# Kernel optimization log

Hardware: AMD Instinct MI355X
Metric: run time of the kernel (lower is better)

Reference implementation:

```python
import jax, jax.numpy as jnp
import numpy as np

N = 200000
E = 1000000
IN_DIM = 16
HID = 64
OUT = 1
EPS = 1e-5


def setup_inputs() -> dict:
    key = jax.random.key(0)
    ks = jax.random.split(key, 24)
    x = jax.random.normal(ks[0], (N, IN_DIM), dtype=jnp.float32)
    edge_index = jax.random.randint(ks[1], (2, E), 0, N, dtype=jnp.int64)

    def lin(k, fan_in, fan_out):
        s = 1.0 / np.sqrt(fan_in)
        return jax.random.uniform(k, (fan_in, fan_out), jnp.float32, -s, s)

    inp = {
        'x': x, 'edge_index': edge_index,
        'W1': lin(ks[2], IN_DIM, HID), 'b1': jnp.zeros((HID,), jnp.float32),
        'W2': lin(ks[3], HID, HID), 'b2': jnp.zeros((HID,), jnp.float32),
        'W3': lin(ks[4], HID, HID), 'b3': jnp.zeros((HID,), jnp.float32),
        'fc_w': lin(ks[5], HID, OUT),
        'fc_b': jnp.zeros((OUT,), jnp.float32),
    }
    # BatchNorm params / running stats (eval mode) — randomized for nontrivial math
    for i, kk in zip((1, 2, 3), range(6, 24, 4)):
        inp[f'g{i}'] = 1.0 + 0.1 * jax.random.normal(ks[kk], (HID,), jnp.float32)
        inp[f'be{i}'] = 0.1 * jax.random.normal(ks[kk + 1], (HID,), jnp.float32)
        inp[f'm{i}'] = 0.1 * jax.random.normal(ks[kk + 2], (HID,), jnp.float32)
        inp[f'v{i}'] = 0.5 + jax.random.uniform(ks[kk + 3], (HID,), jnp.float32)
    return inp


def gcn_conv(x, src, dst, W, b):
    # PyG GCNConv: add self-loops, symmetric normalization, aggregate at dst, bias after aggregation
    h = x @ W                                   # [N, F]
    deg = 1.0 + jax.ops.segment_sum(jnp.ones((E,), x.dtype), dst, num_segments=N)
    dinv = jax.lax.rsqrt(deg)                   # deg >= 1 (self loop)
    norm = dinv[src] * dinv[dst]                # [E]
    msg = h[src] * norm[:, None]                # [E, F] gather + scale
    agg = jax.ops.segment_sum(msg, dst, num_segments=N)
    agg = agg + h * (dinv * dinv)[:, None]      # self-loop contribution
    return agg + b


def bn(x, g, be, m, v):
    return g * (x - m) * jax.lax.rsqrt(v + EPS) + be


def reference(x, edge_index, W1, b1, W2, b2, W3, b3, fc_w, fc_b,
              g1, be1, m1, v1, g2, be2, m2, v2, g3, be3, m3, v3):
    src, dst = edge_index[0], edge_index[1]
    h = jax.nn.relu(bn(gcn_conv(x, src, dst, W1, b1), g1, be1, m1, v1))
    residual = h  # dropout is identity in eval mode
    h = jax.nn.relu(bn(gcn_conv(h, src, dst, W2, b2), g2, be2, m2, v2))
    h = jax.nn.relu(bn(gcn_conv(h, src, dst, W3, b3), g3, be3, m3, v3))
    h = h + residual
    out = h @ fc_w + fc_b
    return jax.nn.sigmoid(out) * 10.0
```

## Files before the change

kernel.cpp:

```cpp
#include <hip/hip_runtime.h>
#include <hip/hip_bf16.h>
#include <math.h>

constexpr int HIDF = 64;

typedef __attribute__((ext_vector_type(8))) short short8;
typedef __attribute__((ext_vector_type(4))) float f32x4;

static inline size_t align_up(size_t x, size_t a) { return (x + a - 1) & ~(a - 1); }

__device__ inline ushort f2bf(float x) {
    __hip_bfloat16 h = __float2bfloat16(x);
    return __builtin_bit_cast(ushort, h);
}
__device__ inline float bflo(unsigned int u) {
    return __builtin_bit_cast(float, u << 16);
}
__device__ inline float bfhi(unsigned int u) {
    return __builtin_bit_cast(float, u & 0xffff0000u);
}
__device__ inline unsigned int pack2(float lo, float hi) {
    return (unsigned int)f2bf(lo) | ((unsigned int)f2bf(hi) << 16);
}


__global__ __launch_bounds__(256) void k_hist(const int* __restrict__ dst,
                                              int* __restrict__ bukcnt,
                                              int ne, int nbuk) {
    __shared__ int lh[512];
    int tid = threadIdx.x;
    lh[tid] = 0; lh[tid + 256] = 0;
    __syncthreads();
#pragma unroll
    for (int k = 0; k < 8; ++k) {
        int idx = blockIdx.x * 2048 + k * 256 + tid;
        if (idx < ne) atomicAdd(&lh[dst[idx] >> 9], 1);
    }
    __syncthreads();
    for (int b = tid; b < nbuk; b += 256) {
        int c = lh[b];
        if (c) atomicAdd(&bukcnt[b], c);
    }
}

__global__ __launch_bounds__(512) void k_bukscan(const int* __restrict__ bukcnt,
                                                 int* __restrict__ bukbase,
                                                 int* __restrict__ gcur,
                                                 int* __restrict__ rowptr,
                                                 int nbuk, int ne, int n) {
    __shared__ int s[512];
    int tid = threadIdx.x;
    int c = (tid < nbuk) ? bukcnt[tid] : 0;
    s[tid] = c;
    __syncthreads();
    for (int off = 1; off < 512; off <<= 1) {
        int t = (tid >= off) ? s[tid - off] : 0;
        __syncthreads();
        s[tid] += t;
        __syncthreads();
    }
    int excl = s[tid] - c;
    if (tid < nbuk) { bukbase[tid] = excl; gcur[tid * 16] = excl; }
    if (tid == 0) { bukbase[nbuk] = ne; rowptr[n] = ne; }
}

__global__ __launch_bounds__(256) void k_scatter_pairs(
    const int* __restrict__ src, const int* __restrict__ dst,
    int* __restrict__ gcur, unsigned* __restrict__ pairs, int ne, int nbuk) {
    __shared__ int lh[512];
    __shared__ int lb[512];
    int tid = threadIdx.x;
    int d[16], sv[16];
#pragma unroll
    for (int k = 0; k < 16; ++k) {
        int idx = blockIdx.x * 4096 + k * 256 + tid;
        bool ok = idx < ne;
        d[k] = ok ? dst[idx] : -1;
        sv[k] = ok ? src[idx] : 0;
    }
    lh[tid] = 0; lh[tid + 256] = 0;
    __syncthreads();
#pragma unroll
    for (int k = 0; k < 16; ++k)
        if (d[k] >= 0) atomicAdd(&lh[d[k] >> 9], 1);
    __syncthreads();
    for (int b = tid; b < nbuk; b += 256) {
        int c = lh[b];
        lb[b] = c ? atomicAdd(&gcur[b * 16], c) : 0;
    }
    __syncthreads();
#pragma unroll
    for (int k = 0; k < 16; ++k)
        if (d[k] >= 0) {
            int pos = atomicAdd(&lb[d[k] >> 9], 1);
            pairs[pos] = (unsigned)sv[k] | ((unsigned)(d[k] & 511) << 18);
        }
}

__global__ __launch_bounds__(512) void k_bucket_sort(
    const unsigned* __restrict__ pairs, const int* __restrict__ bukbase,
    int* __restrict__ rowptr, float* __restrict__ dinv,
    int* __restrict__ esrc, int n) {
    __shared__ int lcnt[512];
    __shared__ int lscan[512];
    __shared__ int lcur[512];
    __shared__ int stage[4096];
    int b = blockIdx.x, tid = threadIdx.x;
    int base = bukbase[b];
    int cnt = bukbase[b + 1] - base;
    lcnt[tid] = 0;
    __syncthreads();
    for (int i = tid; i < cnt; i += 512)
        atomicAdd(&lcnt[pairs[base + i] >> 18], 1);
    __syncthreads();
    int v = lcnt[tid];
    lscan[tid] = v;
    __syncthreads();
    for (int off = 1; off < 512; off <<= 1) {
        int t = (tid >= off) ? lscan[tid - off] : 0;
        __syncthreads();
        lscan[tid] += t;
        __syncthreads();
    }
    int excl = lscan[tid] - v;
    lcur[tid] = excl;
    int node = (b << 9) + tid;
    if (node < n) {
        rowptr[node] = base + excl;
        dinv[node] = rsqrtf(1.f + (float)v);
    }
    __syncthreads();
    for (int i = tid; i < cnt; i += 512) {
        unsigned u = pairs[base + i];
        int p = atomicAdd(&lcur[u >> 18], 1);
        if (p < 4096) stage[p] = (int)(u & 0x3FFFF);
    }
    __syncthreads();
    for (int i = tid; i < cnt && i < 4096; i += 512)
        esrc[base + i] = stage[i];
}

__global__ __launch_bounds__(256) void k_prep(
    const float* __restrict__ W1, const float* __restrict__ W2,
    const float* __restrict__ W3, ushort* __restrict__ wb,
    const float* __restrict__ b1, const float* __restrict__ g1,
    const float* __restrict__ be1, const float* __restrict__ m1, const float* __restrict__ v1,
    const float* __restrict__ b2, const float* __restrict__ g2,
    const float* __restrict__ be2, const float* __restrict__ m2, const float* __restrict__ v2,
    const float* __restrict__ b3, const float* __restrict__ g3,
    const float* __restrict__ be3, const float* __restrict__ m3, const float* __restrict__ v3,
    float* __restrict__ ST) {
    int i = blockIdx.x * 256 + threadIdx.x;
    if (i < 1024) wb[i] = f2bf(W1[i]);
    else if (i < 5120) wb[i] = f2bf(W2[i - 1024]);
    else if (i < 9216) wb[i] = f2bf(W3[i - 5120]);
    int j = i - 9216;
    if (j >= 0 && j < 192) {
        int li = j >> 6, f = j & 63;
        const float* g  = li == 0 ? g1  : li == 1 ? g2  : g3;
        const float* be = li == 0 ? be1 : li == 1 ? be2 : be3;
        const float* m  = li == 0 ? m1  : li == 1 ? m2  : m3;
        const float* v  = li == 0 ? v1  : li == 1 ? v2  : v3;
        const float* bb = li == 0 ? b1  : li == 1 ? b2  : b3;
        float sc = g[f] * rsqrtf(v[f] + 1e-5f);
        ST[li * 128 + f] = sc;
        ST[li * 128 + 64 + f] = sc * (bb[f] - m[f]) + be[f];
    }
}

__global__ __launch_bounds__(256) void k_gemm1(
    const float* __restrict__ X, const ushort* __restrict__ Wb,
    const float* __restrict__ dinv, ushort* __restrict__ hsb, int n) {
    int wid = (blockIdx.x * 256 + threadIdx.x) >> 6;
    int lane = threadIdx.x & 63;
    int lr = lane & 15, lg = lane >> 4;
    int row16 = wid * 16;
    if (row16 >= n) return;

    short8 bf[4];
#pragma unroll
    for (int nt = 0; nt < 4; ++nt) {
        short8 f = {0, 0, 0, 0, 0, 0, 0, 0};
        if (lg < 2)
#pragma unroll
            for (int i = 0; i < 8; ++i)
                f[i] = (short)Wb[(lg * 8 + i) * 64 + nt * 16 + lr];
        bf[nt] = f;
    }

    short8 af = {0, 0, 0, 0, 0, 0, 0, 0};
    if (lg < 2) {
        const float* ar = X + (size_t)(row16 + lr) * 16 + lg * 8;
        float4 u0 = *reinterpret_cast<const float4*>(ar);
        float4 u1 = *reinterpret_cast<const float4*>(ar + 4);
        af[0] = (short)f2bf(u0.x); af[1] = (short)f2bf(u0.y);
        af[2] = (short)f2bf(u0.z); af[3] = (short)f2bf(u0.w);
        af[4] = (short)f2bf(u1.x); af[5] = (short)f2bf(u1.y);
        af[6] = (short)f2bf(u1.z); af[7] = (short)f2bf(u1.w);
    }

    f32x4 acc[4] = {{0, 0, 0, 0}, {0, 0, 0, 0}, {0, 0, 0, 0}, {0, 0, 0, 0}};
#pragma unroll
    for (int nt = 0; nt < 4; ++nt)
        acc[nt] = __builtin_amdgcn_mfma_f32_16x16x32_bf16(af, bf[nt], acc[nt], 0, 0, 0);

#pragma unroll
    for (int j = 0; j < 4; ++j) {
        int row = row16 + lg * 4 + j;
        float di = dinv[row];
#pragma unroll
        for (int nt = 0; nt < 4; ++nt)
            hsb[(size_t)row * 64 + nt * 16 + lr] = f2bf(acc[nt][j] * di);
    }
}

__device__ inline void addrow(float a[8], uint4 u) {
    a[0] += bflo(u.x); a[1] += bfhi(u.x);
    a[2] += bflo(u.y); a[3] += bfhi(u.y);
    a[4] += bflo(u.z); a[5] += bfhi(u.z);
    a[6] += bflo(u.w); a[7] += bfhi(u.w);
}

__device__ inline void agg_core(const uint4* hs4, const int* rowptr,
                                const int* esrc, int node, int q, int lane,
                                float a[8]) {
    addrow(a, hs4[(size_t)node * 8 + q]);
    int start = rowptr[node], deg = rowptr[node + 1] - start;
    int gb = lane & 56;
    int ev = (q < deg) ? esrc[start + q] : 0;
    int it = 0;
    for (; it + 4 <= deg; it += 4) {
        int s0 = (it + 0 < 8) ? __shfl(ev, gb + it + 0, 64) : esrc[start + it + 0];
        int s1 = (it + 1 < 8) ? __shfl(ev, gb + it + 1, 64) : esrc[start + it + 1];
        int s2 = (it + 2 < 8) ? __shfl(ev, gb + it + 2, 64) : esrc[start + it + 2];
        int s3 = (it + 3 < 8) ? __shfl(ev, gb + it + 3, 64) : esrc[start + it + 3];
        uint4 r0 = hs4[(size_t)s0 * 8 + q];
        uint4 r1 = hs4[(size_t)s1 * 8 + q];
        uint4 r2 = hs4[(size_t)s2 * 8 + q];
        uint4 r3 = hs4[(size_t)s3 * 8 + q];
        addrow(a, r0); addrow(a, r1); addrow(a, r2); addrow(a, r3);
    }
    for (; it < deg; ++it) {
        int s = (it < 8) ? __shfl(ev, gb + it, 64) : esrc[start + it];
        addrow(a, hs4[(size_t)s * 8 + q]);
    }
}

template <bool WRITE_H>
__global__ __launch_bounds__(256) void k_agg_gemm(
    const ushort* __restrict__ hsbIn, const int* __restrict__ rowptr,
    const int* __restrict__ esrc, const float* __restrict__ dinv,
    const float* __restrict__ S, const float* __restrict__ T,
    const ushort* __restrict__ Wb, ushort* __restrict__ hb_out,
    ushort* __restrict__ hs_out, int n) {
    __shared__ uint4 hl[8 * 32];
    int tid = threadIdx.x;
    int lane = tid & 63;
    int node0 = blockIdx.x * 32;
    int ln = tid >> 3;
    int node = node0 + ln;
    int q = tid & 7;

    uint4 w = make_uint4(0u, 0u, 0u, 0u);
    if (node < n) {
        float a[8] = {0, 0, 0, 0, 0, 0, 0, 0};
        agg_core(reinterpret_cast<const uint4*>(hsbIn), rowptr, esrc, node, q, lane, a);
        float di = dinv[node];
        const float4* S4 = reinterpret_cast<const float4*>(S);
        const float4* T4 = reinterpret_cast<const float4*>(T);
        float4 sA = S4[q * 2], sB = S4[q * 2 + 1];
        float4 tA = T4[q * 2], tB = T4[q * 2 + 1];
        float o0 = fmaxf(fmaf(sA.x * di, a[0], tA.x), 0.f);
        float o1 = fmaxf(fmaf(sA.y * di, a[1], tA.y), 0.f);
        float o2 = fmaxf(fmaf(sA.z * di, a[2], tA.z), 0.f);
        float o3 = fmaxf(fmaf(sA.w * di, a[3], tA.w), 0.f);
        float o4 = fmaxf(fmaf(sB.x * di, a[4], tB.x), 0.f);
        float o5 = fmaxf(fmaf(sB.y * di, a[5], tB.y), 0.f);
        float o6 = fmaxf(fmaf(sB.z * di, a[6], tB.z), 0.f);
        float o7 = fmaxf(fmaf(sB.w * di, a[7], tB.w), 0.f);
        w.x = pack2(o0, o1); w.y = pack2(o2, o3);
        w.z = pack2(o4, o5); w.w = pack2(o6, o7);
        if (WRITE_H)
            reinterpret_cast<uint4*>(hb_out)[(size_t)node * 8 + q] = w;
    }
    hl[q * 32 + ln] = w;
    __syncthreads();

    int wv = tid >> 6;
    int wr = wv >> 1, wc = wv & 1;
    int lr = lane & 15, lg = lane >> 4;

    short8 af[2];
#pragma unroll
    for (int kt = 0; kt < 2; ++kt)
        af[kt] = __builtin_bit_cast(short8, hl[(kt * 4 + lg) * 32 + wr * 16 + lr]);

    short8 bf[2][2];
#pragma unroll
    for (int nt = 0; nt < 2; ++nt)
#pragma unroll
        for (int kt = 0; kt < 2; ++kt) {
            short8 f;
#pragma unroll
            for (int i = 0; i < 8; ++i)
                f[i] = (short)Wb[(kt * 32 + lg * 8 + i) * 64 + wc * 32 + nt * 16 + lr];
            bf[nt][kt] = f;
        }

    f32x4 acc[2] = {{0, 0, 0, 0}, {0, 0, 0, 0}};
#pragma unroll
    for (int kt = 0; kt < 2; ++kt)
#pragma unroll
        for (int nt = 0; nt < 2; ++nt)
            acc[nt] = __builtin_amdgcn_mfma_f32_16x16x32_bf16(af[kt], bf[nt][kt], acc[nt], 0, 0, 0);

#pragma unroll
    for (int j = 0; j < 4; ++j) {
        int row = node0 + wr * 16 + lg * 4 + j;
        if (row < n) {
            float di = dinv[row];
#pragma unroll
            for (int nt = 0; nt < 2; ++nt)
                hs_out[(size_t)row * 64 + wc * 32 + nt * 16 + lr] = f2bf(acc[nt][j] * di);
        }
    }
}

__global__ __launch_bounds__(256) void k_agg_final(
    const ushort* __restrict__ hsb, const int* __restrict__ rowptr,
    const int* __restrict__ esrc, const float* __restrict__ dinv,
    const float* __restrict__ S, const float* __restrict__ T,
    const ushort* __restrict__ h1, const float* __restrict__ fcw,
    const float* __restrict__ fcb, float* __restrict__ out, int n) {
    int t = blockIdx.x * 256 + threadIdx.x;
    int node = t >> 3;
    if (node >= n) return;
    int q = t & 7, lane = threadIdx.x & 63;
    float a[8] = {0, 0, 0, 0, 0, 0, 0, 0};
    agg_core(reinterpret_cast<const uint4*>(hsb), rowptr, esrc, node, q, lane, a);
    float di = dinv[node];
    const float4* S4 = reinterpret_cast<const float4*>(S);
    const float4* T4 = reinterpret_cast<const float4*>(T);
    float4 sA = S4[q * 2], sB = S4[q * 2 + 1];
    float4 tA = T4[q * 2], tB = T4[q * 2 + 1];
    uint4 r = reinterpret_cast<const uint4*>(h1)[(size_t)node * 8 + q];
    float h0 = fmaxf(fmaf(sA.x * di, a[0], tA.x), 0.f) + bflo(r.x);
    float h1v = fmaxf(fmaf(sA.y * di, a[1], tA.y), 0.f) + bfhi(r.x);
    float h2 = fmaxf(fmaf(sA.z * di, a[2], tA.z), 0.f) + bflo(r.y);
    float h3 = fmaxf(fmaf(sA.w * di, a[3], tA.w), 0.f) + bfhi(r.y);
    float h4 = fmaxf(fmaf(sB.x * di, a[4], tB.x), 0.f) + bflo(r.z);
    float h5 = fmaxf(fmaf(sB.y * di, a[5], tB.y), 0.f) + bfhi(r.z);
    float h6 = fmaxf(fmaf(sB.z * di, a[6], tB.z), 0.f) + bflo(r.w);
    float h7 = fmaxf(fmaf(sB.w * di, a[7], tB.w), 0.f) + bfhi(r.w);
    float4 fA = reinterpret_cast<const float4*>(fcw)[q * 2];
    float4 fB = reinterpret_cast<const float4*>(fcw)[q * 2 + 1];
    float p = h0 * fA.x + h1v * fA.y + h2 * fA.z + h3 * fA.w +
              h4 * fB.x + h5 * fB.y + h6 * fB.z + h7 * fB.w;
    p += __shfl_xor(p, 1, 64);
    p += __shfl_xor(p, 2, 64);
    p += __shfl_xor(p, 4, 64);
    if (q == 0) out[node] = 10.f / (1.f + expf(-(p + fcb[0])));
}

extern "C" void kernel_launch(void* const* d_in, const int* in_sizes, int n_in,
                              void* d_out, int out_size, void* d_ws, size_t ws_size,
                              hipStream_t stream) {
    const float* x   = (const float*)d_in[0];
    const int*   ei  = (const int*)d_in[1];
    const float* W1  = (const float*)d_in[2];
    const float* b1  = (const float*)d_in[3];
    const float* W2  = (const float*)d_in[4];
    const float* b2  = (const float*)d_in[5];
    const float* W3  = (const float*)d_in[6];
    const float* b3  = (const float*)d_in[7];
    const float* fcw = (const float*)d_in[8];
    const float* fcb = (const float*)d_in[9];
    const float* g1 = (const float*)d_in[10], *be1 = (const float*)d_in[11];
    const float* m1 = (const float*)d_in[12], *v1  = (const float*)d_in[13];
    const float* g2 = (const float*)d_in[14], *be2 = (const float*)d_in[15];
    const float* m2 = (const float*)d_in[16], *v2  = (const float*)d_in[17];
    const float* g3 = (const float*)d_in[18], *be3 = (const float*)d_in[19];
    const float* m3 = (const float*)d_in[20], *v3  = (const float*)d_in[21];

    const int N = in_sizes[0] / 16;
    const int E = in_sizes[1] / 2;
    const int* src = ei;
    const int* dst = ei + E;
    float* out = (float*)d_out;

    char* w = (char*)d_ws;
    auto take = [&](size_t bytes) { char* p = w; w += align_up(bytes, 256); return p; };
    float*    dinv    = (float*)take((size_t)N * 4);
    int*      rowptr  = (int*)take((size_t)(N + 1) * 4);
    int*      bukcnt  = (int*)take(512 * 4);
    int*      bukbase = (int*)take(513 * 4);
    int*      gcur    = (int*)take(512 * 16 * 4);
    unsigned* pairs   = (unsigned*)take((size_t)E * 4);
    int*      esrc    = (int*)take((size_t)E * 4);
    ushort*   hsbA    = (ushort*)take((size_t)N * HIDF * 2);
    ushort*   hsbB    = (ushort*)take((size_t)N * HIDF * 2);
    ushort*   h1b     = (ushort*)take((size_t)N * HIDF * 2);
    ushort*   wb      = (ushort*)take((size_t)9216 * 2);
    float*    ST      = (float*)take(3 * 128 * 4);

    const int NBUK  = (N + 511) >> 9;
    const int gHist = (E + 2047) / 2048;
    const int gScat = (E + 4095) / 4096;
    const int gT    = ((N + 15) / 16 * 64 + 255) / 256;
    const int gAG   = (N + 31) / 32;
    const int gAgg  = (N * 8 + 255) / 256;

    hipMemsetAsync(bukcnt, 0, 512 * 4, stream);
    k_hist<<<gHist, 256, 0, stream>>>(dst, bukcnt, E, NBUK);
    k_bukscan<<<1, 512, 0, stream>>>(bukcnt, bukbase, gcur, rowptr, NBUK, E, N);
    k_scatter_pairs<<<gScat, 256, 0, stream>>>(src, dst, gcur, pairs, E, NBUK);
    k_bucket_sort<<<NBUK, 512, 0, stream>>>(pairs, bukbase, rowptr, dinv, esrc, N);

    k_prep<<<37, 256, 0, stream>>>(W1, W2, W3, wb,
                                   b1, g1, be1, m1, v1,
                                   b2, g2, be2, m2, v2,
                                   b3, g3, be3, m3, v3, ST);

    k_gemm1<<<gT, 256, 0, stream>>>(x, wb, dinv, hsbA, N);
    k_agg_gemm<true><<<gAG, 256, 0, stream>>>(hsbA, rowptr, esrc, dinv,
                                              ST, ST + 64, wb + 1024, h1b, hsbB, N);
    k_agg_gemm<false><<<gAG, 256, 0, stream>>>(hsbB, rowptr, esrc, dinv,
                                               ST + 128, ST + 192, wb + 5120, nullptr, hsbA, N);
    k_agg_final<<<gAgg, 256, 0, stream>>>(hsbA, rowptr, esrc, dinv,
                                          ST + 256, ST + 320, h1b, fcw, fcb, out, N);
}
```

Baseline: 255.0 us.

## Fuse weight prep into histogram, vectorize edge loads, add occupancy bounds

```diff
diff --git a/kernel.cpp b/kernel.cpp
--- a/kernel.cpp
+++ b/kernel.cpp
@@ -24,123 +24,8 @@
 }
 
 
-__global__ __launch_bounds__(256) void k_hist(const int* __restrict__ dst,
-                                              int* __restrict__ bukcnt,
-                                              int ne, int nbuk) {
-    __shared__ int lh[512];
-    int tid = threadIdx.x;
-    lh[tid] = 0; lh[tid + 256] = 0;
-    __syncthreads();
-#pragma unroll
-    for (int k = 0; k < 8; ++k) {
-        int idx = blockIdx.x * 2048 + k * 256 + tid;
-        if (idx < ne) atomicAdd(&lh[dst[idx] >> 9], 1);
-    }
-    __syncthreads();
-    for (int b = tid; b < nbuk; b += 256) {
-        int c = lh[b];
-        if (c) atomicAdd(&bukcnt[b], c);
-    }
-}
-
-__global__ __launch_bounds__(512) void k_bukscan(const int* __restrict__ bukcnt,
-                                                 int* __restrict__ bukbase,
-                                                 int* __restrict__ gcur,
-                                                 int* __restrict__ rowptr,
-                                                 int nbuk, int ne, int n) {
-    __shared__ int s[512];
-    int tid = threadIdx.x;
-    int c = (tid < nbuk) ? bukcnt[tid] : 0;
-    s[tid] = c;
-    __syncthreads();
-    for (int off = 1; off < 512; off <<= 1) {
-        int t = (tid >= off) ? s[tid - off] : 0;
-        __syncthreads();
-        s[tid] += t;
-        __syncthreads();
-    }
-    int excl = s[tid] - c;
-    if (tid < nbuk) { bukbase[tid] = excl; gcur[tid * 16] = excl; }
-    if (tid == 0) { bukbase[nbuk] = ne; rowptr[n] = ne; }
-}
-
-__global__ __launch_bounds__(256) void k_scatter_pairs(
-    const int* __restrict__ src, const int* __restrict__ dst,
-    int* __restrict__ gcur, unsigned* __restrict__ pairs, int ne, int nbuk) {
-    __shared__ int lh[512];
-    __shared__ int lb[512];
-    int tid = threadIdx.x;
-    int d[16], sv[16];
-#pragma unroll
-    for (int k = 0; k < 16; ++k) {
-        int idx = blockIdx.x * 4096 + k * 256 + tid;
-        bool ok = idx < ne;
-        d[k] = ok ? dst[idx] : -1;
-        sv[k] = ok ? src[idx] : 0;
-    }
-    lh[tid] = 0; lh[tid + 256] = 0;
-    __syncthreads();
-#pragma unroll
-    for (int k = 0; k < 16; ++k)
-        if (d[k] >= 0) atomicAdd(&lh[d[k] >> 9], 1);
-    __syncthreads();
-    for (int b = tid; b < nbuk; b += 256) {
-        int c = lh[b];
-        lb[b] = c ? atomicAdd(&gcur[b * 16], c) : 0;
-    }
-    __syncthreads();
-#pragma unroll
-    for (int k = 0; k < 16; ++k)
-        if (d[k] >= 0) {
-            int pos = atomicAdd(&lb[d[k] >> 9], 1);
-            pairs[pos] = (unsigned)sv[k] | ((unsigned)(d[k] & 511) << 18);
-        }
-}
-
-__global__ __launch_bounds__(512) void k_bucket_sort(
-    const unsigned* __restrict__ pairs, const int* __restrict__ bukbase,
-    int* __restrict__ rowptr, float* __restrict__ dinv,
-    int* __restrict__ esrc, int n) {
-    __shared__ int lcnt[512];
-    __shared__ int lscan[512];
-    __shared__ int lcur[512];
-    __shared__ int stage[4096];
-    int b = blockIdx.x, tid = threadIdx.x;
-    int base = bukbase[b];
-    int cnt = bukbase[b + 1] - base;
-    lcnt[tid] = 0;
-    __syncthreads();
-    for (int i = tid; i < cnt; i += 512)
-        atomicAdd(&lcnt[pairs[base + i] >> 18], 1);
-    __syncthreads();
-    int v = lcnt[tid];
-    lscan[tid] = v;
-    __syncthreads();
-    for (int off = 1; off < 512; off <<= 1) {
-        int t = (tid >= off) ? lscan[tid - off] : 0;
-        __syncthreads();
-        lscan[tid] += t;
-        __syncthreads();
-    }
-    int excl = lscan[tid] - v;
-    lcur[tid] = excl;
-    int node = (b << 9) + tid;
-    if (node < n) {
-        rowptr[node] = base + excl;
-        dinv[node] = rsqrtf(1.f + (float)v);
-    }
-    __syncthreads();
-    for (int i = tid; i < cnt; i += 512) {
-        unsigned u = pairs[base + i];
-        int p = atomicAdd(&lcur[u >> 18], 1);
-        if (p < 4096) stage[p] = (int)(u & 0x3FFFF);
-    }
-    __syncthreads();
-    for (int i = tid; i < cnt && i < 4096; i += 512)
-        esrc[base + i] = stage[i];
-}
-
-__global__ __launch_bounds__(256) void k_prep(
+__global__ __launch_bounds__(256) void k_hist(
+    const int* __restrict__ dst, int* __restrict__ bukcnt, int ne, int nbuk,
     const float* __restrict__ W1, const float* __restrict__ W2,
     const float* __restrict__ W3, ushort* __restrict__ wb,
     const float* __restrict__ b1, const float* __restrict__ g1,
@@ -150,7 +35,31 @@
     const float* __restrict__ b3, const float* __restrict__ g3,
     const float* __restrict__ be3, const float* __restrict__ m3, const float* __restrict__ v3,
     float* __restrict__ ST) {
-    int i = blockIdx.x * 256 + threadIdx.x;
+    __shared__ int lh[512];
+    int tid = threadIdx.x;
+    lh[tid] = 0; lh[tid + 256] = 0;
+    __syncthreads();
+    const int4* dst4 = reinterpret_cast<const int4*>(dst);
+    int ne4 = ne >> 2;
+#pragma unroll
+    for (int k = 0; k < 2; ++k) {
+        int i = blockIdx.x * 512 + k * 256 + tid;
+        if (i < ne4) {
+            int4 d = dst4[i];
+            atomicAdd(&lh[d.x >> 9], 1);
+            atomicAdd(&lh[d.y >> 9], 1);
+            atomicAdd(&lh[d.z >> 9], 1);
+            atomicAdd(&lh[d.w >> 9], 1);
+        }
+    }
+    if (blockIdx.x == 0 && tid == 0)
+        for (int i = ne4 * 4; i < ne; ++i) atomicAdd(&bukcnt[dst[i] >> 9], 1);
+    __syncthreads();
+    for (int b = tid; b < nbuk; b += 256) {
+        int c = lh[b];
+        if (c) atomicAdd(&bukcnt[b], c);
+    }
+    int i = blockIdx.x * 256 + tid;
     if (i < 1024) wb[i] = f2bf(W1[i]);
     else if (i < 5120) wb[i] = f2bf(W2[i - 1024]);
     else if (i < 9216) wb[i] = f2bf(W3[i - 5120]);
@@ -166,6 +75,116 @@
         ST[li * 128 + f] = sc;
         ST[li * 128 + 64 + f] = sc * (bb[f] - m[f]) + be[f];
     }
+}
+
+__global__ __launch_bounds__(512) void k_bukscan(const int* __restrict__ bukcnt,
+                                                 int* __restrict__ bukbase,
+                                                 int* __restrict__ gcur,
+                                                 int* __restrict__ rowptr,
+                                                 int nbuk, int ne, int n) {
+    __shared__ int s[512];
+    int tid = threadIdx.x;
+    int c = (tid < nbuk) ? bukcnt[tid] : 0;
+    s[tid] = c;
+    __syncthreads();
+    for (int off = 1; off < 512; off <<= 1) {
+        int t = (tid >= off) ? s[tid - off] : 0;
+        __syncthreads();
+        s[tid] += t;
+        __syncthreads();
+    }
+    int excl = s[tid] - c;
+    if (tid < nbuk) { bukbase[tid] = excl; gcur[tid * 16] = excl; }
+    if (tid == 0) { bukbase[nbuk] = ne; rowptr[n] = ne; }
+}
+
+__global__ __launch_bounds__(256) void k_scatter_pairs(
+    const int* __restrict__ src, const int* __restrict__ dst,
+    int* __restrict__ gcur, unsigned* __restrict__ pairs, int ne, int nbuk) {
+    __shared__ int lh[512];
+    __shared__ int lb[512];
+    int tid = threadIdx.x;
+    const int4* src4 = reinterpret_cast<const int4*>(src);
+    const int4* dst4 = reinterpret_cast<const int4*>(dst);
+    int ne4 = ne >> 2;
+    int4 d[4], sv[4];
+#pragma unroll
+    for (int k = 0; k < 4; ++k) {
+        int i = blockIdx.x * 1024 + k * 256 + tid;
+        bool ok = i < ne4;
+        d[k] = ok ? dst4[i] : make_int4(-1, -1, -1, -1);
+        sv[k] = ok ? src4[i] : make_int4(0, 0, 0, 0);
+    }
+    lh[tid] = 0; lh[tid + 256] = 0;
+    __syncthreads();
+#pragma unroll
+    for (int k = 0; k < 4; ++k) {
+        if (d[k].x >= 0) atomicAdd(&lh[d[k].x >> 9], 1);
+        if (d[k].y >= 0) atomicAdd(&lh[d[k].y >> 9], 1);
+        if (d[k].z >= 0) atomicAdd(&lh[d[k].z >> 9], 1);
+        if (d[k].w >= 0) atomicAdd(&lh[d[k].w >> 9], 1);
+    }
+    __syncthreads();
+    for (int b = tid; b < nbuk; b += 256) {
+        int c = lh[b];
+        lb[b] = c ? atomicAdd(&gcur[b * 16], c) : 0;
+    }
+    __syncthreads();
+#pragma unroll
+    for (int k = 0; k < 4; ++k) {
+        if (d[k].x >= 0) { int p = atomicAdd(&lb[d[k].x >> 9], 1); pairs[p] = (unsigned)sv[k].x | ((unsigned)(d[k].x & 511) << 18); }
+        if (d[k].y >= 0) { int p = atomicAdd(&lb[d[k].y >> 9], 1); pairs[p] = (unsigned)sv[k].y | ((unsigned)(d[k].y & 511) << 18); }
+        if (d[k].z >= 0) { int p = atomicAdd(&lb[d[k].z >> 9], 1); pairs[p] = (unsigned)sv[k].z | ((unsigned)(d[k].z & 511) << 18); }
+        if (d[k].w >= 0) { int p = atomicAdd(&lb[d[k].w >> 9], 1); pairs[p] = (unsigned)sv[k].w | ((unsigned)(d[k].w & 511) << 18); }
+    }
+    if (blockIdx.x == 0 && tid == 0)
+        for (int i = ne4 * 4; i < ne; ++i) {
+            int p = atomicAdd(&gcur[(dst[i] >> 9) * 16], 1);
+            pairs[p] = (unsigned)src[i] | ((unsigned)(dst[i] & 511) << 18);
+        }
+}
+
+__global__ __launch_bounds__(512) void k_bucket_sort(
+    const unsigned* __restrict__ pairs, const int* __restrict__ bukbase,
+    int* __restrict__ rowptr, float* __restrict__ dinv,
+    int* __restrict__ esrc, int n) {
+    __shared__ int lcnt[512];
+    __shared__ int lscan[512];
+    __shared__ int lcur[512];
+    __shared__ int stage[4096];
+    int b = blockIdx.x, tid = threadIdx.x;
+    int base = bukbase[b];
+    int cnt = bukbase[b + 1] - base;
+    lcnt[tid] = 0;
+    __syncthreads();
+    for (int i = tid; i < cnt; i += 512)
+        atomicAdd(&lcnt[pairs[base + i] >> 18], 1);
+    __syncthreads();
+    int v = lcnt[tid];
+    lscan[tid] = v;
+    __syncthreads();
+    for (int off = 1; off < 512; off <<= 1) {
+        int t = (tid >= off) ? lscan[tid - off] : 0;
+        __syncthreads();
+        lscan[tid] += t;
+        __syncthreads();
+    }
+    int excl = lscan[tid] - v;
+    lcur[tid] = excl;
+    int node = (b << 9) + tid;
+    if (node < n) {
+        rowptr[node] = base + excl;
+        dinv[node] = rsqrtf(1.f + (float)v);
+    }
+    __syncthreads();
+    for (int i = tid; i < cnt; i += 512) {
+        unsigned u = pairs[base + i];
+        int p = atomicAdd(&lcur[u >> 18], 1);
+        if (p < 4096) stage[p] = (int)(u & 0x3FFFF);
+    }
+    __syncthreads();
+    for (int i = tid; i < cnt && i < 4096; i += 512)
+        esrc[base + i] = stage[i];
 }
 
 __global__ __launch_bounds__(256) void k_gemm1(
@@ -247,7 +266,7 @@
 }
 
 template <bool WRITE_H>
-__global__ __launch_bounds__(256) void k_agg_gemm(
+__global__ __launch_bounds__(256, 6) void k_agg_gemm(
     const ushort* __restrict__ hsbIn, const int* __restrict__ rowptr,
     const int* __restrict__ esrc, const float* __restrict__ dinv,
     const float* __restrict__ S, const float* __restrict__ T,
@@ -326,7 +345,7 @@
     }
 }
 
-__global__ __launch_bounds__(256) void k_agg_final(
+__global__ __launch_bounds__(256, 8) void k_agg_final(
     const ushort* __restrict__ hsb, const int* __restrict__ rowptr,
     const int* __restrict__ esrc, const float* __restrict__ dinv,
     const float* __restrict__ S, const float* __restrict__ T,
@@ -404,22 +423,21 @@
     float*    ST      = (float*)take(3 * 128 * 4);
 
     const int NBUK  = (N + 511) >> 9;
-    const int gHist = (E + 2047) / 2048;
-    const int gScat = (E + 4095) / 4096;
+    const int gHist = ((E >> 2) + 511) / 512;
+    const int gScat = ((E >> 2) + 1023) / 1024;
     const int gT    = ((N + 15) / 16 * 64 + 255) / 256;
     const int gAG   = (N + 31) / 32;
     const int gAgg  = (N * 8 + 255) / 256;
 
     hipMemsetAsync(bukcnt, 0, 512 * 4, stream);
-    k_hist<<<gHist, 256, 0, stream>>>(dst, bukcnt, E, NBUK);
+    k_hist<<<gHist, 256, 0, stream>>>(dst, bukcnt, E, NBUK,
+                                      W1, W2, W3, wb,
+                                      b1, g1, be1, m1, v1,
+                                      b2, g2, be2, m2, v2,
+                                      b3, g3, be3, m3, v3, ST);
     k_bukscan<<<1, 512, 0, stream>>>(bukcnt, bukbase, gcur, rowptr, NBUK, E, N);
     k_scatter_pairs<<<gScat, 256, 0, stream>>>(src, dst, gcur, pairs, E, NBUK);
     k_bucket_sort<<<NBUK, 512, 0, stream>>>(pairs, bukbase, rowptr, dinv, esrc, N);
-
-    k_prep<<<37, 256, 0, stream>>>(W1, W2, W3, wb,
-                                   b1, g1, be1, m1, v1,
-                                   b2, g2, be2, m2, v2,
-                                   b3, g3, be3, m3, v3, ST);
 
     k_gemm1<<<gT, 256, 0, stream>>>(x, wb, dinv, hsbA, N);
     k_agg_gemm<true><<<gAG, 256, 0, stream>>>(hsbA, rowptr, esrc, dinv,
```

Result: faster. 249.6 us (-2.1%).
